# Performance work log

Hardware: AMD Instinct MI355X
Metric: run time of the kernel (lower is better)

Reference implementation:

```python
import jax, jax.numpy as jnp
import numpy as np

N_NODES = 5200    # max node index bounded by EW_weight length (5200)
N_INCID = 5200    # hyperedge_index.size(1), bounded by EW_weight length
N_HEDGES = 1000   # bounded by hyperedge_weight parameter length
N_DIM = 4096
NEG_SLOPE = 0.01  # torch.nn.LeakyReLU() default


def setup_inputs() -> dict:
    key = jax.random.key(0)
    k1, k2, k3, k4, k5, k6 = jax.random.split(key, 6)
    node_idx = jax.random.randint(k1, (N_INCID,), 0, N_NODES, dtype=jnp.int32)
    edge_idx = jax.random.randint(k2, (N_INCID,), 0, N_HEDGES, dtype=jnp.int32)
    edge_idx = edge_idx.at[-1].set(N_HEDGES - 1)  # ensure num_edges = max+1 = N_HEDGES (static)
    hyperedge_index = jnp.stack([node_idx, edge_idx], axis=0)
    features = jax.random.normal(k3, (N_NODES, N_DIM), dtype=jnp.float32)
    hyperedge_type = jnp.round(jax.random.uniform(k4, (N_HEDGES, 1), dtype=jnp.float32))
    return {
        "features": features,
        "hyperedge_index": hyperedge_index,
        "hyperedge_type": hyperedge_type,
        "hyperedge_weight": jnp.ones((1000,), jnp.float32),
        "hyperedge_attr1": jax.random.uniform(k5, (N_DIM,), dtype=jnp.float32),
        "hyperedge_attr2": jax.random.uniform(k6, (N_DIM,), dtype=jnp.float32),
        "EW_weight": jnp.ones((5200,), jnp.float32),
        "bias": jnp.zeros((N_DIM,), jnp.float32),
    }


def reference(features, hyperedge_index, hyperedge_type, hyperedge_weight,
              hyperedge_attr1, hyperedge_attr2, EW_weight, bias):
    node_idx = hyperedge_index[0]  # [E] node index of each incidence
    edge_idx = hyperedge_index[1]  # [E] hyperedge index of each incidence
    E = node_idx.shape[0]

    hw = hyperedge_weight[:N_HEDGES]   # hgnn slices param to num_edges
    norm = EW_weight[:E]               # hgnn slices param to E, passed as EW_weight

    # hyperedge_attr is computed but unused (use_attention=False in source)
    _ = hyperedge_attr1 * hyperedge_type + hyperedge_attr2 * (1.0 - hyperedge_type)

    # D: node-degree normalization (sum of incident hyperedge weights per node)
    D = jax.ops.segment_sum(hw[edge_idx], node_idx, num_segments=N_NODES)
    Dinv = jnp.where(D == 0, 0.0, 1.0 / D)
    # B: hyperedge normalization (sum of EW weights of member nodes per edge)
    B = jax.ops.segment_sum(norm[node_idx], edge_idx, num_segments=N_HEDGES)
    Binv = jnp.where(B == 0, 0.0, 1.0 / B)

    # Stage 1: node -> hyperedge (flow source_to_target), message = B_e * x_v
    msg1 = Binv[edge_idx][:, None] * features[node_idx]           # [E, F]
    edge_out = jax.ops.segment_sum(msg1, edge_idx, num_segments=N_HEDGES)  # [num_edges, F]

    # Stage 2: hyperedge -> node (flow target_to_source), message = D_v * e_feat
    msg2 = Dinv[node_idx][:, None] * edge_out[edge_idx]           # [E, F]
    node_out = jax.ops.segment_sum(msg2, node_idx, num_segments=N_NODES)   # [N, F]

    node_out = node_out + bias
    return (jax.nn.leaky_relu(node_out, NEG_SLOPE),
            jax.nn.leaky_relu(edge_out, NEG_SLOPE))
```

## Files before the change

### kernel.cpp

```cpp
#include <hip/hip_runtime.h>

#define NN 5200
#define NI 5200
#define NH 1000
#define ND 4096
#define SLOPE 0.01f
#define INV_SLOPE 100.0f
#define EBK 64
#define NBK 16

__global__ void __launch_bounds__(256) edge_k(const float* __restrict__ feat,
        const int* __restrict__ hidx, const float* __restrict__ eww,
        float* __restrict__ eout) {
    __shared__ int cnt;
    __shared__ float Bs;
    __shared__ int list[EBK];
    const int h = blockIdx.x, t = threadIdx.x;
    if (t == 0) { cnt = 0; Bs = 0.f; }
    __syncthreads();
    for (int i = t; i < NI; i += 256) {
        if (hidx[NI + i] == h) {
            int n = hidx[i];
            int p = atomicAdd(&cnt, 1);
            if (p < EBK) list[p] = n;
            atomicAdd(&Bs, eww[n]);
        }
    }
    __syncthreads();
    int c = cnt < EBK ? cnt : EBK;
    float B = Bs;
    float binv = (B == 0.f) ? 0.f : 1.f / B;

    float4 a0 = make_float4(0.f, 0.f, 0.f, 0.f), a1 = a0, a2 = a0, a3 = a0;
    for (int j = 0; j < c; ++j) {
        const float4* row = (const float4*)(feat + (size_t)list[j] * ND);
        float4 v0 = row[t], v1 = row[t + 256], v2 = row[t + 512], v3 = row[t + 768];
        a0.x += v0.x; a0.y += v0.y; a0.z += v0.z; a0.w += v0.w;
        a1.x += v1.x; a1.y += v1.y; a1.z += v1.z; a1.w += v1.w;
        a2.x += v2.x; a2.y += v2.y; a2.z += v2.z; a2.w += v2.w;
        a3.x += v3.x; a3.y += v3.y; a3.z += v3.z; a3.w += v3.w;
    }
    float4* out = (float4*)(eout + (size_t)h * ND);
#define EFIN(ak, idx)                                              \
    {                                                              \
        float4 r;                                                  \
        r.x = binv * ak.x; r.y = binv * ak.y;                      \
        r.z = binv * ak.z; r.w = binv * ak.w;                      \
        r.x = r.x >= 0.f ? r.x : SLOPE * r.x;                      \
        r.y = r.y >= 0.f ? r.y : SLOPE * r.y;                      \
        r.z = r.z >= 0.f ? r.z : SLOPE * r.z;                      \
        r.w = r.w >= 0.f ? r.w : SLOPE * r.w;                      \
        out[idx] = r;                                              \
    }
    EFIN(a0, t) EFIN(a1, t + 256) EFIN(a2, t + 512) EFIN(a3, t + 768)
#undef EFIN
}

__global__ void __launch_bounds__(256) node_k(const float* __restrict__ eout,
        const int* __restrict__ hidx, const float* __restrict__ hw,
        const float* __restrict__ bias, float* __restrict__ nout) {
    __shared__ int cnt;
    __shared__ float Ds;
    __shared__ int list[NBK];
    const int n = blockIdx.x, t = threadIdx.x;
    if (t == 0) { cnt = 0; Ds = 0.f; }
    __syncthreads();
    for (int i = t; i < NI; i += 256) {
        if (hidx[i] == n) {
            int h = hidx[NI + i];
            int p = atomicAdd(&cnt, 1);
            if (p < NBK) list[p] = h;
            atomicAdd(&Ds, hw[h]);
        }
    }
    __syncthreads();
    int c = cnt < NBK ? cnt : NBK;
    float D = Ds;
    float dinv = (D == 0.f) ? 0.f : 1.f / D;

    float4 a0 = make_float4(0.f, 0.f, 0.f, 0.f), a1 = a0, a2 = a0, a3 = a0;
    for (int j = 0; j < c; ++j) {
        const float4* row = (const float4*)(eout + (size_t)list[j] * ND);
        float4 v0 = row[t], v1 = row[t + 256], v2 = row[t + 512], v3 = row[t + 768];
        v0.x = v0.x >= 0.f ? v0.x : INV_SLOPE * v0.x;
        v0.y = v0.y >= 0.f ? v0.y : INV_SLOPE * v0.y;
        v0.z = v0.z >= 0.f ? v0.z : INV_SLOPE * v0.z;
        v0.w = v0.w >= 0.f ? v0.w : INV_SLOPE * v0.w;
        v1.x = v1.x >= 0.f ? v1.x : INV_SLOPE * v1.x;
        v1.y = v1.y >= 0.f ? v1.y : INV_SLOPE * v1.y;
        v1.z = v1.z >= 0.f ? v1.z : INV_SLOPE * v1.z;
        v1.w = v1.w >= 0.f ? v1.w : INV_SLOPE * v1.w;
        v2.x = v2.x >= 0.f ? v2.x : INV_SLOPE * v2.x;
        v2.y = v2.y >= 0.f ? v2.y : INV_SLOPE * v2.y;
        v2.z = v2.z >= 0.f ? v2.z : INV_SLOPE * v2.z;
        v2.w = v2.w >= 0.f ? v2.w : INV_SLOPE * v2.w;
        v3.x = v3.x >= 0.f ? v3.x : INV_SLOPE * v3.x;
        v3.y = v3.y >= 0.f ? v3.y : INV_SLOPE * v3.y;
        v3.z = v3.z >= 0.f ? v3.z : INV_SLOPE * v3.z;
        v3.w = v3.w >= 0.f ? v3.w : INV_SLOPE * v3.w;
        a0.x += v0.x; a0.y += v0.y; a0.z += v0.z; a0.w += v0.w;
        a1.x += v1.x; a1.y += v1.y; a1.z += v1.z; a1.w += v1.w;
        a2.x += v2.x; a2.y += v2.y; a2.z += v2.z; a2.w += v2.w;
        a3.x += v3.x; a3.y += v3.y; a3.z += v3.z; a3.w += v3.w;
    }
    const float4* b4 = (const float4*)bias;
    float4* out = (float4*)(nout + (size_t)n * ND);
#define NFIN(ak, idx)                                              \
    {                                                              \
        float4 b = b4[idx];                                        \
        float4 v;                                                  \
        v.x = dinv * ak.x + b.x; v.y = dinv * ak.y + b.y;          \
        v.z = dinv * ak.z + b.z; v.w = dinv * ak.w + b.w;          \
        v.x = v.x >= 0.f ? v.x : SLOPE * v.x;                      \
        v.y = v.y >= 0.f ? v.y : SLOPE * v.y;                      \
        v.z = v.z >= 0.f ? v.z : SLOPE * v.z;                      \
        v.w = v.w >= 0.f ? v.w : SLOPE * v.w;                      \
        out[idx] = v;                                              \
    }
    NFIN(a0, t) NFIN(a1, t + 256) NFIN(a2, t + 512) NFIN(a3, t + 768)
#undef NFIN
}

extern "C" void kernel_launch(void* const* d_in, const int* in_sizes, int n_in,
                              void* d_out, int out_size, void* d_ws, size_t ws_size,
                              hipStream_t stream) {
    const float* feat = (const float*)d_in[0];
    const int* hidx   = (const int*)d_in[1];
    const float* hw   = (const float*)d_in[3];
    const float* eww  = (const float*)d_in[6];
    const float* bias = (const float*)d_in[7];

    float* nout = (float*)d_out;
    float* eout = nout + (size_t)NN * ND;

    edge_k<<<NH, 256, 0, stream>>>(feat, hidx, eww, eout);
    node_k<<<NN, 256, 0, stream>>>(eout, hidx, hw, bias, nout);
}
```

Baseline: 204.1 us.

## Precompute incidence buckets and degree sums in a separate build kernel

Adds a build kernel that scatters each incidence into per-edge and per-node bucket lists and accumulates the B and D sums with global atomics. Before this, every edge block and node block scanned the whole 5200-entry index array, about 6200 full scans in total. The edge and node kernels now only read their own precomputed bucket. The change also uses nontemporal loads for the feature rows and nontemporal stores for the node output. It costs a memset and an extra launch, and bucket order now depends on atomic ordering, so float summation order is nondeterministic.

```diff
diff --git a/kernel.cpp b/kernel.cpp
--- a/kernel.cpp
+++ b/kernel.cpp
@@ -9,43 +9,48 @@
 #define EBK 64
 #define NBK 16
 
+typedef float v4f __attribute__((ext_vector_type(4)));
+
+__global__ void build_k(const int* __restrict__ hidx, const float* __restrict__ hw,
+                        const float* __restrict__ eww,
+                        int* __restrict__ ecnt, int* __restrict__ ncnt,
+                        float* __restrict__ Bsum, float* __restrict__ Dsum,
+                        int* __restrict__ ebuk, int* __restrict__ nbuk) {
+    int i = blockIdx.x * blockDim.x + threadIdx.x;
+    if (i < NI) {
+        int n = hidx[i];
+        int h = hidx[NI + i];
+        int q = atomicAdd(&ecnt[h], 1);
+        if (q < EBK) ebuk[h * EBK + q] = n;
+        int p = atomicAdd(&ncnt[n], 1);
+        if (p < NBK) nbuk[n * NBK + p] = h;
+        atomicAdd(&Bsum[h], eww[n]);
+        atomicAdd(&Dsum[n], hw[h]);
+    }
+}
+
 __global__ void __launch_bounds__(256) edge_k(const float* __restrict__ feat,
-        const int* __restrict__ hidx, const float* __restrict__ eww,
-        float* __restrict__ eout) {
-    __shared__ int cnt;
-    __shared__ float Bs;
-    __shared__ int list[EBK];
+        const int* __restrict__ ecnt, const float* __restrict__ Bsum,
+        const int* __restrict__ ebuk, float* __restrict__ eout) {
     const int h = blockIdx.x, t = threadIdx.x;
-    if (t == 0) { cnt = 0; Bs = 0.f; }
-    __syncthreads();
-    for (int i = t; i < NI; i += 256) {
-        if (hidx[NI + i] == h) {
-            int n = hidx[i];
-            int p = atomicAdd(&cnt, 1);
-            if (p < EBK) list[p] = n;
-            atomicAdd(&Bs, eww[n]);
-        }
-    }
-    __syncthreads();
-    int c = cnt < EBK ? cnt : EBK;
-    float B = Bs;
+    int c = ecnt[h];
+    if (c > EBK) c = EBK;
+    float B = Bsum[h];
     float binv = (B == 0.f) ? 0.f : 1.f / B;
 
-    float4 a0 = make_float4(0.f, 0.f, 0.f, 0.f), a1 = a0, a2 = a0, a3 = a0;
+    v4f a0 = (v4f)(0.f), a1 = a0, a2 = a0, a3 = a0;
     for (int j = 0; j < c; ++j) {
-        const float4* row = (const float4*)(feat + (size_t)list[j] * ND);
-        float4 v0 = row[t], v1 = row[t + 256], v2 = row[t + 512], v3 = row[t + 768];
-        a0.x += v0.x; a0.y += v0.y; a0.z += v0.z; a0.w += v0.w;
-        a1.x += v1.x; a1.y += v1.y; a1.z += v1.z; a1.w += v1.w;
-        a2.x += v2.x; a2.y += v2.y; a2.z += v2.z; a2.w += v2.w;
-        a3.x += v3.x; a3.y += v3.y; a3.z += v3.z; a3.w += v3.w;
+        const v4f* row = (const v4f*)(feat + (size_t)ebuk[h * EBK + j] * ND);
+        v4f v0 = __builtin_nontemporal_load(row + t);
+        v4f v1 = __builtin_nontemporal_load(row + t + 256);
+        v4f v2 = __builtin_nontemporal_load(row + t + 512);
+        v4f v3 = __builtin_nontemporal_load(row + t + 768);
+        a0 += v0; a1 += v1; a2 += v2; a3 += v3;
     }
-    float4* out = (float4*)(eout + (size_t)h * ND);
+    v4f* out = (v4f*)(eout + (size_t)h * ND);
 #define EFIN(ak, idx)                                              \
     {                                                              \
-        float4 r;                                                  \
-        r.x = binv * ak.x; r.y = binv * ak.y;                      \
-        r.z = binv * ak.z; r.w = binv * ak.w;                      \
+        v4f r = binv * ak;                                         \
         r.x = r.x >= 0.f ? r.x : SLOPE * r.x;                      \
         r.y = r.y >= 0.f ? r.y : SLOPE * r.y;                      \
         r.z = r.z >= 0.f ? r.z : SLOPE * r.z;                      \
@@ -57,65 +62,38 @@
 }
 
 __global__ void __launch_bounds__(256) node_k(const float* __restrict__ eout,
-        const int* __restrict__ hidx, const float* __restrict__ hw,
-        const float* __restrict__ bias, float* __restrict__ nout) {
-    __shared__ int cnt;
-    __shared__ float Ds;
-    __shared__ int list[NBK];
+        const int* __restrict__ ncnt, const float* __restrict__ Dsum,
+        const int* __restrict__ nbuk, const float* __restrict__ bias,
+        float* __restrict__ nout) {
     const int n = blockIdx.x, t = threadIdx.x;
-    if (t == 0) { cnt = 0; Ds = 0.f; }
-    __syncthreads();
-    for (int i = t; i < NI; i += 256) {
-        if (hidx[i] == n) {
-            int h = hidx[NI + i];
-            int p = atomicAdd(&cnt, 1);
-            if (p < NBK) list[p] = h;
-            atomicAdd(&Ds, hw[h]);
-        }
-    }
-    __syncthreads();
-    int c = cnt < NBK ? cnt : NBK;
-    float D = Ds;
+    int c = ncnt[n];
+    if (c > NBK) c = NBK;
+    float D = Dsum[n];
     float dinv = (D == 0.f) ? 0.f : 1.f / D;
 
-    float4 a0 = make_float4(0.f, 0.f, 0.f, 0.f), a1 = a0, a2 = a0, a3 = a0;
+    v4f a0 = (v4f)(0.f), a1 = a0, a2 = a0, a3 = a0;
+#define IREL(vk)                                                   \
+    vk.x = vk.x >= 0.f ? vk.x : INV_SLOPE * vk.x;                  \
+    vk.y = vk.y >= 0.f ? vk.y : INV_SLOPE * vk.y;                  \
+    vk.z = vk.z >= 0.f ? vk.z : INV_SLOPE * vk.z;                  \
+    vk.w = vk.w >= 0.f ? vk.w : INV_SLOPE * vk.w;
     for (int j = 0; j < c; ++j) {
-        const float4* row = (const float4*)(eout + (size_t)list[j] * ND);
-        float4 v0 = row[t], v1 = row[t + 256], v2 = row[t + 512], v3 = row[t + 768];
-        v0.x = v0.x >= 0.f ? v0.x : INV_SLOPE * v0.x;
-        v0.y = v0.y >= 0.f ? v0.y : INV_SLOPE * v0.y;
-        v0.z = v0.z >= 0.f ? v0.z : INV_SLOPE * v0.z;
-        v0.w = v0.w >= 0.f ? v0.w : INV_SLOPE * v0.w;
-        v1.x = v1.x >= 0.f ? v1.x : INV_SLOPE * v1.x;
-        v1.y = v1.y >= 0.f ? v1.y : INV_SLOPE * v1.y;
-        v1.z = v1.z >= 0.f ? v1.z : INV_SLOPE * v1.z;
-        v1.w = v1.w >= 0.f ? v1.w : INV_SLOPE * v1.w;
-        v2.x = v2.x >= 0.f ? v2.x : INV_SLOPE * v2.x;
-        v2.y = v2.y >= 0.f ? v2.y : INV_SLOPE * v2.y;
-        v2.z = v2.z >= 0.f ? v2.z : INV_SLOPE * v2.z;
-        v2.w = v2.w >= 0.f ? v2.w : INV_SLOPE * v2.w;
-        v3.x = v3.x >= 0.f ? v3.x : INV_SLOPE * v3.x;
-        v3.y = v3.y >= 0.f ? v3.y : INV_SLOPE * v3.y;
-        v3.z = v3.z >= 0.f ? v3.z : INV_SLOPE * v3.z;
-        v3.w = v3.w >= 0.f ? v3.w : INV_SLOPE * v3.w;
-        a0.x += v0.x; a0.y += v0.y; a0.z += v0.z; a0.w += v0.w;
-        a1.x += v1.x; a1.y += v1.y; a1.z += v1.z; a1.w += v1.w;
-        a2.x += v2.x; a2.y += v2.y; a2.z += v2.z; a2.w += v2.w;
-        a3.x += v3.x; a3.y += v3.y; a3.z += v3.z; a3.w += v3.w;
+        const v4f* row = (const v4f*)(eout + (size_t)nbuk[n * NBK + j] * ND);
+        v4f v0 = row[t], v1 = row[t + 256], v2 = row[t + 512], v3 = row[t + 768];
+        IREL(v0) IREL(v1) IREL(v2) IREL(v3)
+        a0 += v0; a1 += v1; a2 += v2; a3 += v3;
     }
-    const float4* b4 = (const float4*)bias;
-    float4* out = (float4*)(nout + (size_t)n * ND);
+#undef IREL
+    const v4f* b4 = (const v4f*)bias;
+    v4f* out = (v4f*)(nout + (size_t)n * ND);
 #define NFIN(ak, idx)                                              \
     {                                                              \
-        float4 b = b4[idx];                                        \
-        float4 v;                                                  \
-        v.x = dinv * ak.x + b.x; v.y = dinv * ak.y + b.y;          \
-        v.z = dinv * ak.z + b.z; v.w = dinv * ak.w + b.w;          \
+        v4f v = dinv * ak + b4[idx];                               \
         v.x = v.x >= 0.f ? v.x : SLOPE * v.x;                      \
         v.y = v.y >= 0.f ? v.y : SLOPE * v.y;                      \
         v.z = v.z >= 0.f ? v.z : SLOPE * v.z;                      \
         v.w = v.w >= 0.f ? v.w : SLOPE * v.w;                      \
-        out[idx] = v;                                              \
+        __builtin_nontemporal_store(v, out + idx);                 \
     }
     NFIN(a0, t) NFIN(a1, t + 256) NFIN(a2, t + 512) NFIN(a3, t + 768)
 #undef NFIN
@@ -133,6 +111,17 @@
     float* nout = (float*)d_out;
     float* eout = nout + (size_t)NN * ND;
 
-    edge_k<<<NH, 256, 0, stream>>>(feat, hidx, eww, eout);
-    node_k<<<NN, 256, 0, stream>>>(eout, hidx, hw, bias, nout);
+    int* ws     = (int*)d_ws;
+    int* ecnt   = ws;
+    int* ncnt   = ecnt + NH;
+    float* Bsum = (float*)(ncnt + NN);
+    float* Dsum = Bsum + NH;
+    int* ebuk   = (int*)(Dsum + NN);
+    int* nbuk   = ebuk + NH * EBK;
+
+    (void)hipMemsetAsync(ecnt, 0, (size_t)2 * (NH + NN) * sizeof(int), stream);
+    build_k<<<(NI + 255) / 256, 256, 0, stream>>>(hidx, hw, eww, ecnt, ncnt,
+                                                  Bsum, Dsum, ebuk, nbuk);
+    edge_k<<<NH, 256, 0, stream>>>(feat, ecnt, Bsum, ebuk, eout);
+    node_k<<<NN, 256, 0, stream>>>(eout, ncnt, Dsum, nbuk, bias, nout);
 }
```

New measurement: 193.3 us. 1.06x faster.
